# Performance work log

Hardware: AMD Instinct MI355X
Metric: run time of the kernel (lower is better)

Reference implementation:

```python
import jax, jax.numpy as jnp
import numpy as np

B, N, TD, SD, BD, K, M, TOPK, H = 8, 1024, 5120, 2048, 1024, 16, 4, 2, 8
HD = SD // H  # 256


def _ln(x, g, b, eps=1e-5):
    m = jnp.mean(x, -1, keepdims=True)
    v = jnp.mean((x - m) ** 2, -1, keepdims=True)
    return (x - m) * jax.lax.rsqrt(v + eps) * g + b


def _adapter(h, dw, db, uw, ub, lg, lb, q, wq, bq, wk, bk, wv, bv, ow, ob, pg, pb):
    # bottleneck trunk: down -> GELU -> up -> LN (dropout = identity in eval)
    x = jax.nn.gelu(h @ dw + db, approximate=False)          # [B,N,BD]
    x = _ln(x @ uw + ub, lg, lb)                             # [B,N,SD]
    Bb = x.shape[0]
    # cross-attention: learnable queries [K,SD] attend over x
    qp = (q @ wq + bq).reshape(K, H, HD).transpose(1, 0, 2)                      # [H,K,HD]
    kp = (x @ wk + bk).reshape(Bb, -1, H, HD).transpose(0, 2, 1, 3)              # [B,H,N,HD]
    vp = (x @ wv + bv).reshape(Bb, -1, H, HD).transpose(0, 2, 1, 3)              # [B,H,N,HD]
    att = jax.nn.softmax(jnp.einsum('hkd,bhnd->bhkn', qp, kp) * (1.0 / np.sqrt(HD)), axis=-1)
    ctx = jnp.einsum('bhkn,bhnd->bhkd', att, vp).transpose(0, 2, 1, 3).reshape(Bb, K, SD)
    ctx = ctx @ ow + ob
    return _ln(ctx + q[None], pg, pb)                        # residual with queries


def setup_inputs():
    key = jax.random.key(0)
    it = iter(jax.random.split(key, 40))
    def nrm(shape, s=0.02):
        return jax.random.normal(next(it), shape, jnp.float32) * s
    inp = {'h_teacher': jax.random.normal(next(it), (B, N, TD), jnp.float32)}
    for pre, lead in (('g_', ()), ('s_', (M,))):
        inp[pre + 'dw'] = nrm(lead + (TD, BD)); inp[pre + 'db'] = jnp.zeros(lead + (BD,), jnp.float32)
        inp[pre + 'uw'] = nrm(lead + (BD, SD)); inp[pre + 'ub'] = jnp.zeros(lead + (SD,), jnp.float32)
        inp[pre + 'lg'] = jnp.ones(lead + (SD,), jnp.float32); inp[pre + 'lb'] = jnp.zeros(lead + (SD,), jnp.float32)
        inp[pre + 'q'] = nrm(lead + (K, SD))
        for nm in ('wq', 'wk', 'wv', 'ow'):
            inp[pre + nm] = nrm(lead + (SD, SD))
        for nm in ('bq', 'bk', 'bv', 'ob'):
            inp[pre + nm] = jnp.zeros(lead + (SD,), jnp.float32)
        inp[pre + 'pg'] = jnp.ones(lead + (SD,), jnp.float32); inp[pre + 'pb'] = jnp.zeros(lead + (SD,), jnp.float32)
    inp['r_w1'] = nrm((TD, 512)); inp['r_b1'] = jnp.zeros((512,), jnp.float32)
    inp['r_w2'] = nrm((512, M)); inp['r_b2'] = jnp.zeros((M,), jnp.float32)
    return inp


def reference(h_teacher, g_dw, g_db, g_uw, g_ub, g_lg, g_lb, g_q, g_wq, g_bq, g_wk, g_bk, g_wv, g_bv, g_ow, g_ob, g_pg, g_pb, s_dw, s_db, s_uw, s_ub, s_lg, s_lb, s_q, s_wq, s_bq, s_wk, s_bk, s_wv, s_bv, s_ow, s_ob, s_pg, s_pb, r_w1, r_b1, r_w2, r_b2):
    # generalized adapter (always on)
    c_g = _adapter(h_teacher, g_dw, g_db, g_uw, g_ub, g_lg, g_lb, g_q, g_wq, g_bq, g_wk, g_bk, g_wv, g_bv, g_ow, g_ob, g_pg, g_pb)
    # all specialized experts computed densely (as the torch module does), then gathered
    c_spec = jax.vmap(lambda dw, db, uw, ub, lg, lb, q, wq, bq, wk, bk, wv, bv, ow, ob, pg, pb:
                      _adapter(h_teacher, dw, db, uw, ub, lg, lb, q, wq, bq, wk, bk, wv, bv, ow, ob, pg, pb))(
        s_dw, s_db, s_uw, s_ub, s_lg, s_lb, s_q, s_wq, s_bq, s_wk, s_bk, s_wv, s_bv, s_ow, s_ob, s_pg, s_pb)  # [M,B,K,SD]
    cs = jnp.transpose(c_spec, (1, 0, 2, 3))                 # [B,M,K,SD]
    # router on mean-pooled teacher summary (eval: no noise)
    pooled = jnp.mean(h_teacher, axis=1)                     # [B,TD]
    logits = jax.nn.gelu(pooled @ r_w1 + r_b1, approximate=False) @ r_w2 + r_b2
    probs = jax.nn.softmax(logits, axis=-1)                  # [B,M]
    w, idx = jax.lax.top_k(probs, TOPK)                      # [B,TOPK]
    w = w / (jnp.sum(w, -1, keepdims=True) + 1e-8)
    sel = cs[jnp.arange(cs.shape[0])[:, None], idx]          # [B,TOPK,K,SD]
    c_s = jnp.sum(sel * w[:, :, None, None], axis=1)         # [B,K,SD]
    c_agg = jnp.concatenate([c_g, c_s], axis=1)              # [B,2K,SD]
    return c_agg, probs
```

## Files before the change

### kernel.cpp

```cpp
#include <hip/hip_runtime.h>
#include <hip/hip_bf16.h>

#define B_   8
#define N_   1024
#define TD_  5120
#define SD_  2048
#define BD_  1024
#define K_   16
#define H_   8

typedef unsigned short u16;
typedef __attribute__((ext_vector_type(8))) short bf16x8;
typedef __attribute__((ext_vector_type(4))) float f32x4;
typedef __attribute__((ext_vector_type(8))) u16 u16x8;
typedef __attribute__((ext_vector_type(4))) u16 u16x4;

__device__ __forceinline__ float bf2f(u16 u) {
    union { unsigned int i; float f; } x; x.i = ((unsigned)u) << 16; return x.f;
}
__device__ __forceinline__ u16 f2bf(float f) {
    union { float f; unsigned int i; } x; x.f = f;
    unsigned int i = x.i;
    return (u16)((i + 0x7fffu + ((i >> 16) & 1u)) >> 16);
}
__device__ __forceinline__ float gelu_exact(float v) {
    return 0.5f * v * (1.0f + erff(v * 0.70710678118654752f));
}
__device__ __forceinline__ void gload_lds16(const void* g, void* l) {
    __builtin_amdgcn_global_load_lds(
        (const __attribute__((address_space(1))) unsigned int*)g,
        (__attribute__((address_space(3))) unsigned int*)l, 16, 0, 0);
}

struct Ptr5 { const float* p[5]; };
struct Ptr40 { const float* p[8][5]; };

template<int EPI, int AMODE>
__global__ __launch_bounds__(256, 4)
void gemm128(const u16* __restrict__ Abase,
             const u16* __restrict__ Bbase, long bStride,
             const float* __restrict__ biasBase, int biasStride,
             u16* __restrict__ Cbase, int ldc, long cStride, int Kd,
             const int* __restrict__ units_a, const int* __restrict__ units_b)
{
    __shared__ char lds[32768];
    const int u = blockIdx.z;
    const int ua = units_a[u];
    const int ub = (AMODE == 0) ? units_b[u] : u;
    const u16* A  = Abase + (size_t)ub * 1024 * Kd;
    const u16* Bt = Bbase + (size_t)ua * bStride;
    const float* bias = biasBase + (size_t)ua * biasStride;
    u16* C = Cbase + (size_t)u * cStride;

    const int tid  = threadIdx.x;
    const int wave = tid >> 6, lane = tid & 63;
    const int wm = wave >> 1, wn = wave & 1;
    const int row0 = blockIdx.x * 128, col0 = blockIdx.y * 128;

    const int srow = tid >> 3;
    const int scol = ((tid & 7) ^ (srow & 7)) << 3;
    const char* aSrc = (const char*)(A  + (size_t)(row0 + srow) * Kd + scol);
    const char* bSrc = (const char*)(Bt + (size_t)(col0 + srow) * Kd + scol);
    const int ldsW = wave * 1024;

    const int fr = lane & 15, fq = lane >> 4;
    const int kl  = fq << 4;
    const int swz = (fr & 7) << 4;

    f32x4 acc[4][4] = {};

#define LDA_(mf, kk) (*(const bf16x8*)(lds + \
    (wm*64 + (mf)*16 + fr)*128 + ((((kk)*64) + kl) ^ swz)))
#define LDB_(nf, kk) (*(const bf16x8*)(lds + 16384 + \
    (wn*64 + (nf)*16 + fr)*128 + ((((kk)*64) + kl) ^ swz)))

    const int nt = Kd >> 6;
    for (int T = 0; T < nt; ++T) {
        const size_t kb = (size_t)T << 7;
#pragma unroll
        for (int l = 0; l < 4; ++l)
            gload_lds16(aSrc + (size_t)(l*32)*Kd*2 + kb, lds + l*4096 + ldsW);
#pragma unroll
        for (int l = 0; l < 4; ++l)
            gload_lds16(bSrc + (size_t)(l*32)*Kd*2 + kb, lds + 16384 + l*4096 + ldsW);
        asm volatile("s_waitcnt vmcnt(0)" ::: "memory");
        __syncthreads();
#pragma unroll
        for (int kk = 0; kk < 2; ++kk) {
            bf16x8 aF[4], bF[4];
#pragma unroll
            for (int i = 0; i < 4; ++i) aF[i] = LDA_(i, kk);
#pragma unroll
            for (int n = 0; n < 4; ++n) bF[n] = LDB_(n, kk);
#pragma unroll
            for (int i = 0; i < 4; ++i)
#pragma unroll
                for (int n = 0; n < 4; ++n)
                    acc[i][n] = __builtin_amdgcn_mfma_f32_16x16x32_bf16(
                        aF[i], bF[n], acc[i][n], 0, 0, 0);
        }
        __syncthreads();
    }

#undef LDA_
#undef LDB_

#pragma unroll
    for (int mf = 0; mf < 4; ++mf)
#pragma unroll
        for (int nf = 0; nf < 4; ++nf) {
            const int col = col0 + wn*64 + nf*16 + fr;
            const float bv = bias[col];
#pragma unroll
            for (int j = 0; j < 4; ++j) {
                const int row = row0 + wm*64 + mf*16 + fq*4 + j;
                float v = acc[mf][nf][j] + bv;
                if (EPI == 1) v = gelu_exact(v);
                C[(size_t)row*ldc + col] = f2bf(v);
            }
        }
}

template<int EPI, int AMODE>
__global__ __launch_bounds__(512, 2)
void gemm256(const u16* __restrict__ Abase,
             const u16* __restrict__ Bbase, long bStride,
             const float* __restrict__ biasBase, int biasStride,
             u16* __restrict__ Cbase, int ldc, long cStride, int Kd,
             const int* __restrict__ units_a, const int* __restrict__ units_b)
{
    __shared__ char lds[131072];
    const int u = blockIdx.z;
    const int ua = units_a[u];
    const int ub = (AMODE == 0) ? units_b[u] : u;
    const u16* A  = Abase + (size_t)ub * 1024 * Kd;
    const u16* Bt = Bbase + (size_t)ua * bStride;
    const float* bias = biasBase + (size_t)ua * biasStride;
    u16* C = Cbase + (size_t)u * cStride;

    const int tid  = threadIdx.x;
    const int wave = tid >> 6, lane = tid & 63;
    const int wm = wave >> 2, wn = wave & 3;
    const int row0 = blockIdx.x * 256, col0 = blockIdx.y * 256;

    const int srow = tid >> 3;
    const int scol = ((tid & 7) ^ ((tid >> 3) & 7)) << 3;
    const char* aSrc = (const char*)(A  + (size_t)(row0 + srow) * Kd + scol);
    const char* bSrc = (const char*)(Bt + (size_t)(col0 + srow) * Kd + scol);
    const int ldsW = wave * 1024;

    const int fr = lane & 15, fq = lane >> 4;
    const int kl  = fq << 4;
    const int swz = (fr & 7) << 4;

    f32x4 acc[8][4] = {};
    bf16x8 aF[8], bF[4];

#define STAGE_A(bufv, hh, kt) do { \
    const char* s_ = aSrc + ((size_t)((hh)*128) * Kd + (size_t)(kt) * 64) * 2; \
    char* d_ = lds + (bufv)*65536 + (hh)*16384 + ldsW; \
    gload_lds16(s_, d_); \
    gload_lds16(s_ + (size_t)64 * Kd * 2, d_ + 8192); } while(0)
#define STAGE_B(bufv, hh, kt) do { \
    const char* s_ = bSrc + ((size_t)((hh)*128) * Kd + (size_t)(kt) * 64) * 2; \
    char* d_ = lds + (bufv)*65536 + 32768 + (hh)*16384 + ldsW; \
    gload_lds16(s_, d_); \
    gload_lds16(s_ + (size_t)64 * Kd * 2, d_ + 8192); } while(0)

#define LDA_(bufv, mf, kk) (*(const bf16x8*)(lds + (bufv)*65536 + \
    ((mf)*32 + wm*16 + fr)*128 + ((((kk)*64) + kl) ^ swz)))
#define LDB_(bufv, nf, kk) (*(const bf16x8*)(lds + (bufv)*65536 + 32768 + \
    (wn*64 + (nf)*16 + fr)*128 + ((((kk)*64) + kl) ^ swz)))

#define FENCE_ asm volatile("" ::: "memory")
#define BAR_   __builtin_amdgcn_s_barrier()
#define WAITL_ asm volatile("s_waitcnt lgkmcnt(0)" ::: "memory")
#define VM_(n) asm volatile("s_waitcnt vmcnt(" #n ")" ::: "memory")

#define READ_B(bufv, kk) { _Pragma("unroll") \
    for (int n_ = 0; n_ < 4; ++n_) bF[n_] = LDB_(bufv, n_, kk); }
#define READ_A8(bufv, kk) { _Pragma("unroll") \
    for (int i_ = 0; i_ < 8; ++i_) aF[i_] = LDA_(bufv, i_, kk); }
#define MFMA32_ { __builtin_amdgcn_s_setprio(1); \
    _Pragma("unroll") for (int i_ = 0; i_ < 8; ++i_) { \
      _Pragma("unroll") for (int n_ = 0; n_ < 4; ++n_) \
        acc[i_][n_] = __builtin_amdgcn_mfma_f32_16x16x32_bf16( \
            aF[i_], bF[n_], acc[i_][n_], 0, 0, 0); } \
    __builtin_amdgcn_s_setprio(0); }

    STAGE_A(0, 0, 0); STAGE_A(0, 1, 0);
    STAGE_B(0, 0, 0); STAGE_B(0, 1, 0);

    const int nt = Kd >> 6;
    for (int T = 0; T < nt - 1; ++T) {
        const int bufv = T & 1, nb = bufv ^ 1;
        STAGE_A(nb, 0, T + 1); STAGE_A(nb, 1, T + 1);
        VM_(4); BAR_; FENCE_;
        READ_B(bufv, 0); READ_A8(bufv, 0);
        STAGE_B(nb, 0, T + 1); STAGE_B(nb, 1, T + 1);
        WAITL_; MFMA32_;
        READ_B(bufv, 1); READ_A8(bufv, 1);
        WAITL_; MFMA32_;
        BAR_;
    }
    {
        const int bufv = (nt - 1) & 1;
        VM_(0); BAR_; FENCE_;
        READ_B(bufv, 0); READ_A8(bufv, 0);
        WAITL_; MFMA32_;
        READ_B(bufv, 1); READ_A8(bufv, 1);
        WAITL_; MFMA32_;
    }

#undef STAGE_A
#undef STAGE_B
#undef LDA_
#undef LDB_
#undef FENCE_
#undef BAR_
#undef WAITL_
#undef VM_
#undef READ_B
#undef READ_A8
#undef MFMA32_

#pragma unroll
    for (int mf = 0; mf < 8; ++mf)
#pragma unroll
        for (int nf = 0; nf < 4; ++nf) {
            const int col = col0 + wn*64 + nf*16 + fr;
            const float bv = bias[col];
#pragma unroll
            for (int j = 0; j < 4; ++j) {
                const int row = row0 + mf*32 + wm*16 + fq*4 + j;
                float v = acc[mf][nf][j] + bv;
                if (EPI == 1) v = gelu_exact(v);
                C[(size_t)row*ldc + col] = f2bf(v);
            }
        }
}

__global__ __launch_bounds__(256)
void cvt_pool(const float* __restrict__ h, u16* __restrict__ hb,
              float* __restrict__ pp) {
    const int b = blockIdx.x, nc = blockIdx.y, t = threadIdx.x;
    const float* hp = h + ((size_t)b*N_ + (size_t)nc*8)*TD_;
    u16* op = hb + ((size_t)b*N_ + (size_t)nc*8)*TD_;
    f32x4 sum[5] = {};
    for (int r = 0; r < 8; ++r) {
        const float* rp = hp + (size_t)r*TD_;
        u16* orow = op + (size_t)r*TD_;
#pragma unroll
        for (int j = 0; j < 5; ++j) {
            const int c = (t + 256*j) << 2;
            f32x4 v = *(const f32x4*)(rp + c);
            sum[j] += v;
            u16x4 o = { f2bf(v[0]), f2bf(v[1]), f2bf(v[2]), f2bf(v[3]) };
            *(u16x4*)(orow + c) = o;
        }
    }
#pragma unroll
    for (int j = 0; j < 5; ++j) {
        const int c = (t + 256*j) << 2;
        *(f32x4*)(pp + ((size_t)b*128 + nc)*TD_ + c) = sum[j];
    }
}

__global__ void pool_reduce(const float* __restrict__ pp, float* __restrict__ pooled) {
    const int idx = blockIdx.x*256 + threadIdx.x;
    const int b = idx / TD_, c = idx % TD_;
    float s = 0.f;
    for (int nc = 0; nc < 128; ++nc) s += pp[((size_t)b*128 + nc)*TD_ + c];
    pooled[idx] = s * (1.0f/N_);
}

__global__ __launch_bounds__(256)
void cvt_transpose5(Ptr5 W5, u16* __restrict__ WtBase, long wtStride,
                    int Kd, int Nd) {
    __shared__ float t[64][65];
    const float* W = W5.p[blockIdx.z];
    u16* Wt = WtBase + (size_t)blockIdx.z * wtStride;
    const int k0 = blockIdx.x * 64, n0 = blockIdx.y * 64;
    const int tid = threadIdx.x;
#pragma unroll
    for (int i = 0; i < 4; ++i) {
        int ch = tid + i*256;
        int r = ch >> 4, c4 = (ch & 15) << 2;
        f32x4 v = *(const f32x4*)(W + (size_t)(k0 + r)*Nd + n0 + c4);
        t[r][c4] = v[0]; t[r][c4+1] = v[1]; t[r][c4+2] = v[2]; t[r][c4+3] = v[3];
    }
    __syncthreads();
#pragma unroll
    for (int i = 0; i < 2; ++i) {
        int ch = tid + i*256;
        int nr = ch >> 3, c8 = (ch & 7) << 3;
        u16x8 o;
#pragma unroll
        for (int j = 0; j < 8; ++j) o[j] = f2bf(t[c8 + j][nr]);
        *(u16x8*)(Wt + (size_t)(n0 + nr)*Kd + k0 + c8) = o;
    }
}

__global__ __launch_bounds__(256)
void ln_rows_u(u16* __restrict__ X, const float* __restrict__ gslab,
               const float* __restrict__ bslab, const int* __restrict__ units_a) {
    const int row = blockIdx.x, tid = threadIdx.x;
    const int ua = units_a[row >> 10];
    const float* g  = gslab + (size_t)ua*SD_;
    const float* bt = bslab + (size_t)ua*SD_;
    u16* rp = X + (size_t)row*SD_;
    const u16x8 v = ((const u16x8*)rp)[tid];
    float f[8]; float s = 0.f, s2 = 0.f;
#pragma unroll
    for (int j = 0; j < 8; ++j) { f[j] = bf2f(v[j]); s += f[j]; s2 += f[j]*f[j]; }
    __shared__ float sa[4], sb[4];
#pragma unroll
    for (int o = 32; o > 0; o >>= 1) { s += __shfl_down(s, o); s2 += __shfl_down(s2, o); }
    if ((tid & 63) == 0) { sa[tid >> 6] = s; sb[tid >> 6] = s2; }
    __syncthreads();
    s = sa[0]+sa[1]+sa[2]+sa[3]; s2 = sb[0]+sb[1]+sb[2]+sb[3];
    const float mean = s * (1.0f/SD_);
    const float inv  = rsqrtf(s2 * (1.0f/SD_) - mean*mean + 1e-5f);
    const int c0 = tid*8;
    u16x8 o;
#pragma unroll
    for (int j = 0; j < 8; ++j) o[j] = f2bf((f[j]-mean)*inv*g[c0+j] + bt[c0+j]);
    ((u16x8*)rp)[tid] = o;
}

__global__ __launch_bounds__(256)
void qp_part(Ptr5 q, Ptr5 wq, float* __restrict__ Sp) {
    __shared__ float qL[16][256];
    const int a = blockIdx.y, ks = blockIdx.z;
    const int c = blockIdx.x*256 + threadIdx.x;
    const int t = threadIdx.x;
    const float* Q = q.p[a];
    for (int i = t; i < 16*256; i += 256)
        qL[i >> 8][i & 255] = Q[(size_t)(i >> 8)*SD_ + ks*256 + (i & 255)];
    __syncthreads();
    const float* W = wq.p[a] + (size_t)(ks*256)*SD_ + c;
    float acc[16] = {};
    for (int i = 0; i < 256; i += 4) {
        const float w0 = W[(size_t)i*SD_];
        const float w1 = W[(size_t)(i+1)*SD_];
        const float w2 = W[(size_t)(i+2)*SD_];
        const float w3 = W[(size_t)(i+3)*SD_];
#pragma unroll
        for (int k = 0; k < 16; ++k) {
            f32x4 q4 = *(const f32x4*)&qL[k][i];
            acc[k] += q4[0]*w0 + q4[1]*w1 + q4[2]*w2 + q4[3]*w3;
        }
    }
#pragma unroll
    for (int k = 0; k < 16; ++k)
        Sp[((size_t)(a*8 + ks)*16 + k)*SD_ + c] = acc[k];
}

__global__ void qp_reduce(const float* __restrict__ Sp, Ptr5 bq, float* __restrict__ qp) {
    const int idx = blockIdx.x*256 + threadIdx.x;
    const int a = idx >> 15, k = (idx >> 11) & 15, c = idx & 2047;
    float s = bq.p[a][c];
#pragma unroll
    for (int ks = 0; ks < 8; ++ks)
        s += Sp[((size_t)(a*8 + ks)*16 + k)*SD_ + c];
    qp[idx] = s;
}

__global__ __launch_bounds__(256)
void scores_sm(const u16* __restrict__ Kb, const float* __restrict__ qp,
               const int* __restrict__ units_a, float* __restrict__ P)
{
    __shared__ float sL[16][1024];
    __shared__ float qL[16][256];
    __shared__ float red[8];
    const int u = blockIdx.x >> 3, hh = blockIdx.x & 7;
    const int ua = units_a[u];
    const int t = threadIdx.x;
    for (int i = t; i < 16*256; i += 256)
        qL[i >> 8][i & 255] = qp[(size_t)(ua*16 + (i >> 8))*SD_ + hh*256 + (i & 255)];
    __syncthreads();
    const u16* Ku = Kb + (size_t)u*1024*SD_ + hh*256;
#pragma unroll
    for (int j = 0; j < 4; ++j) {
        const int n = t + j*256;
        const u16* kr = Ku + (size_t)n*SD_;
        float acc[16] = {};
        for (int d0 = 0; d0 < 256; d0 += 8) {
            u16x8 kv8 = *(const u16x8*)(kr + d0);
            float kf[8];
#pragma unroll
            for (int e = 0; e < 8; ++e) kf[e] = bf2f(kv8[e]);
#pragma unroll
            for (int k = 0; k < 16; ++k) {
                f32x4 q0 = *(const f32x4*)&qL[k][d0];
                f32x4 q1 = *(const f32x4*)&qL[k][d0+4];
                acc[k] += q0[0]*kf[0] + q0[1]*kf[1] + q0[2]*kf[2] + q0[3]*kf[3]
                        + q1[0]*kf[4] + q1[1]*kf[5] + q1[2]*kf[6] + q1[3]*kf[7];
            }
        }
#pragma unroll
        for (int k = 0; k < 16; ++k) sL[k][n] = acc[k] * 0.0625f;
    }
    __syncthreads();
    const int lane = t & 63, wv = t >> 6;
    for (int k = 0; k < 16; ++k) {
        float v0 = sL[k][t], v1 = sL[k][t+256], v2 = sL[k][t+512], v3 = sL[k][t+768];
        float mx = fmaxf(fmaxf(v0,v1), fmaxf(v2,v3));
#pragma unroll
        for (int o = 1; o < 64; o <<= 1) mx = fmaxf(mx, __shfl_xor(mx, o));
        if (lane == 0) red[wv] = mx;
        __syncthreads();
        mx = fmaxf(fmaxf(red[0],red[1]), fmaxf(red[2],red[3]));
        float e0 = expf(v0-mx), e1 = expf(v1-mx), e2 = expf(v2-mx), e3 = expf(v3-mx);
        float s = e0+e1+e2+e3;
#pragma unroll
        for (int o = 1; o < 64; o <<= 1) s += __shfl_xor(s, o);
        if (lane == 0) red[4+wv] = s;
        __syncthreads();
        s = red[4]+red[5]+red[6]+red[7];
        const float inv = 1.0f/s;
        float* Pr = P + ((size_t)(u*8+hh)*16 + k)*1024;
        Pr[t]=e0*inv; Pr[t+256]=e1*inv; Pr[t+512]=e2*inv; Pr[t+768]=e3*inv;
        __syncthreads();
    }
}

__global__ __launch_bounds__(256)
void ctx_u(const u16* __restrict__ Vb, const float* __restrict__ P,
           u16* __restrict__ ctxb)
{
    __shared__ float pL[16][1024];
    const int u = blockIdx.x >> 3, hh = blockIdx.x & 7;
    const int t = threadIdx.x;
    const float* Pu = P + (size_t)(u*8+hh)*16*1024;
    for (int i = t; i < 16*1024/4; i += 256)
        ((f32x4*)&pL[0][0])[i] = ((const f32x4*)Pu)[i];
    __syncthreads();
    const u16* Vu = Vb + (size_t)u*1024*SD_ + hh*256 + t;
    float acc[16] = {};
    for (int n = 0; n < 1024; n += 4) {
        float vv0 = bf2f(Vu[(size_t)n*SD_]);
        float vv1 = bf2f(Vu[(size_t)(n+1)*SD_]);
        float vv2 = bf2f(Vu[(size_t)(n+2)*SD_]);
        float vv3 = bf2f(Vu[(size_t)(n+3)*SD_]);
#pragma unroll
        for (int k = 0; k < 16; ++k) {
            f32x4 p4 = *(const f32x4*)&pL[k][n];
            acc[k] += p4[0]*vv0 + p4[1]*vv1 + p4[2]*vv2 + p4[3]*vv3;
        }
    }
#pragma unroll
    for (int k = 0; k < 16; ++k)
        ctxb[(size_t)u*16*SD_ + k*SD_ + hh*256 + t] = f2bf(acc[k]);
}

__global__ __launch_bounds__(256)
void gemm_ow_part(const u16* __restrict__ ctxb, const u16* __restrict__ Bslab,
                  const int* __restrict__ units_a, float* __restrict__ ctx2p)
{
    const int u = blockIdx.y, ua = units_a[u], ks = blockIdx.z;
    const int wave = threadIdx.x >> 6, lane = threadIdx.x & 63;
    const int col0 = blockIdx.x*256 + wave*64;
    const u16* A  = ctxb + (size_t)u*16*SD_;
    const u16* Bt = Bslab + (size_t)ua*SD_*SD_;
    const int fr = lane & 15, fk8 = (lane >> 4) << 3;
    f32x4 acc[4] = {};
    const int kbase = ks*512;
    for (int k0 = kbase; k0 < kbase + 512; k0 += 32) {
        bf16x8 af = *(const bf16x8*)(A + (size_t)fr*SD_ + k0 + fk8);
#pragma unroll
        for (int n = 0; n < 4; ++n) {
            bf16x8 bf8 = *(const bf16x8*)(Bt + (size_t)(col0 + n*16 + fr)*SD_ + k0 + fk8);
            acc[n] = __builtin_amdgcn_mfma_f32_16x16x32_bf16(af, bf8, acc[n], 0, 0, 0);
        }
    }
    const int fq = lane >> 4;
#pragma unroll
    for (int n = 0; n < 4; ++n)
#pragma unroll
        for (int j = 0; j < 4; ++j) {
            const int row = fq*4 + j, col = col0 + n*16 + fr;
            ctx2p[(((size_t)ks*24 + u)*16 + row)*SD_ + col] = acc[n][j];
        }
}

__global__ void gemm_ow_reduce(const float* __restrict__ ctx2p,
                               const float* __restrict__ biasSlab,
                               const int* __restrict__ units_a,
                               float* __restrict__ ctx2) {
    const int idx = blockIdx.x*256 + threadIdx.x;
    const int u = idx / (16*SD_);
    const int rem = idx % (16*SD_);
    const int col = rem % SD_;
    float s = biasSlab[units_a[u]*SD_ + col];
#pragma unroll
    for (int ks = 0; ks < 4; ++ks)
        s += ctx2p[((size_t)ks*24*16*SD_) + (size_t)u*16*SD_ + rem];
    ctx2[idx] = s;
}

__global__ __launch_bounds__(256)
void ln_post_u(const float* __restrict__ ctx2, const float* __restrict__ qslab,
               const float* __restrict__ pgs, const float* __restrict__ pbs,
               const int* __restrict__ units_a, const int* __restrict__ units_b,
               float* __restrict__ out, float* __restrict__ cspec)
{
    const int k = blockIdx.x, u = blockIdx.y, tid = threadIdx.x;
    const int ua = units_a[u];
    const float* ip = ctx2 + ((size_t)u*16 + k)*SD_;
    const float* qr = qslab + ((size_t)ua*16 + k)*SD_;
    const float* g  = pgs + (size_t)ua*SD_;
    const float* bt = pbs + (size_t)ua*SD_;
    float f[8]; float s = 0.f, s2 = 0.f;
#pragma unroll
    for (int j = 0; j < 8; ++j) {
        const int c = tid + j*256;
        f[j] = ip[c] + qr[c];
        s += f[j]; s2 += f[j]*f[j];
    }
    __shared__ float sa[4], sb[4];
#pragma unroll
    for (int o = 32; o > 0; o >>= 1) { s += __shfl_down(s, o); s2 += __shfl_down(s2, o); }
    if ((tid & 63) == 0) { sa[tid >> 6] = s; sb[tid >> 6] = s2; }
    __syncthreads();
    s = sa[0]+sa[1]+sa[2]+sa[3]; s2 = sb[0]+sb[1]+sb[2]+sb[3];
    const float mean = s * (1.0f/SD_);
    const float inv  = rsqrtf(s2 * (1.0f/SD_) - mean*mean + 1e-5f);
    float* op = (u < 8) ? out + ((size_t)units_b[u]*32 + k)*SD_
                        : cspec + ((size_t)(u-8)*16 + k)*SD_;
#pragma unroll
    for (int j = 0; j < 8; ++j) { const int c = tid + j*256; op[c] = (f[j]-mean)*inv*g[c] + bt[c]; }
}

__global__ __launch_bounds__(256)
void rmlp_part(const float* __restrict__ pooled, const float* __restrict__ w1,
               float* __restrict__ rp) {
    const int c = blockIdx.x*256 + threadIdx.x;
    const int b = blockIdx.y, is = blockIdx.z;
    const float* pr = pooled + b*TD_ + is*512;
    const float* W = w1 + (size_t)(is*512)*512 + c;
    float s = 0.f;
    for (int i = 0; i < 512; ++i) s += pr[i] * W[(size_t)i*512];
    rp[(b*10 + is)*512 + c] = s;
}
__global__ void rmlp_reduce(const float* __restrict__ rp, const float* __restrict__ b1,
                            float* __restrict__ hid) {
    const int idx = blockIdx.x*256 + threadIdx.x;
    const int b = idx >> 9, c = idx & 511;
    float s = b1[c];
#pragma unroll
    for (int is = 0; is < 10; ++is) s += rp[(b*10 + is)*512 + c];
    hid[idx] = gelu_exact(s);
}

__global__ void router_final(const float* __restrict__ hid, const float* __restrict__ w2,
                             const float* __restrict__ b2, float* __restrict__ probs,
                             int* __restrict__ widx, float* __restrict__ wval,
                             int* __restrict__ units_a, int* __restrict__ units_b) {
    __shared__ float lg[8][4];
    __shared__ int sw[16];
    const int tid = threadIdx.x;
    if (tid < 32) {
        const int b = tid >> 2, m = tid & 3;
        float s = b2[m];
        const float* hr = hid + b*512;
        for (int i = 0; i < 512; ++i) s += hr[i]*w2[i*4 + m];
        lg[b][m] = s;
    }
    __syncthreads();
    if (tid < 8) {
        const int b = tid;
        const float l0=lg[b][0], l1=lg[b][1], l2=lg[b][2], l3=lg[b][3];
        const float mx = fmaxf(fmaxf(l0,l1),fmaxf(l2,l3));
        const float e0=expf(l0-mx), e1=expf(l1-mx), e2=expf(l2-mx), e3=expf(l3-mx);
        const float s = e0+e1+e2+e3;
        float p[4] = {e0/s, e1/s, e2/s, e3/s};
        probs[b*4+0]=p[0]; probs[b*4+1]=p[1]; probs[b*4+2]=p[2]; probs[b*4+3]=p[3];
        int i0 = 0;
        for (int m = 1; m < 4; ++m) if (p[m] > p[i0]) i0 = m;
        int i1 = -1;
        for (int m = 0; m < 4; ++m) if (m != i0 && (i1 < 0 || p[m] > p[i1])) i1 = m;
        const float w0 = p[i0], w1 = p[i1], ws = w0 + w1 + 1e-8f;
        widx[b*2]=i0; widx[b*2+1]=i1;
        wval[b*2]=w0/ws; wval[b*2+1]=w1/ws;
        sw[b*2]=i0; sw[b*2+1]=i1;
    }
    __syncthreads();
    if (tid < 24) {
        units_a[tid] = (tid < 8) ? 0 : sw[tid-8] + 1;
        units_b[tid] = (tid < 8) ? tid : ((tid-8) >> 1);
    }
}

__global__ void combine_k(const float* __restrict__ cspec, const int* __restrict__ widx,
                          const float* __restrict__ wval, float* __restrict__ out) {
    const int i = blockIdx.x*256 + threadIdx.x;
    const int c4 = i & 511;
    const int k  = (i >> 9) & 15;
    const int b  = i >> 13;
    const float w0 = wval[b*2], w1 = wval[b*2+1];
    const f32x4 v0 = ((const f32x4*)cspec)[(size_t)((2*b)  *16 + k)*512 + c4];
    const f32x4 v1 = ((const f32x4*)cspec)[(size_t)((2*b+1)*16 + k)*512 + c4];
    ((f32x4*)out)[(size_t)(b*32 + 16 + k)*512 + c4] = v0*w0 + v1*w1;
}

__global__ void pack5(Ptr5 src, float* __restrict__ dst, int len) {
    int i = blockIdx.x*256 + threadIdx.x;
    if (i < 5*len) dst[i] = src.p[i/len][i%len];
}
__global__ void pack_slab8(Ptr40 s, float* __restrict__ dst) {
    int i = blockIdx.x*256 + threadIdx.x;
    int slab = i / 10240, rem = i % 10240;
    dst[i] = s.p[slab][rem / 2048][rem % 2048];
}

extern "C" void kernel_launch(void* const* d_in, const int* in_sizes, int n_in,
                              void* d_out, int out_size, void* d_ws, size_t ws_size,
                              hipStream_t stream) {
    if (ws_size < 300300000ULL) return;

    const float* h = (const float*)d_in[0];
    const float* G[17]; const float* Sx[17];
    for (int i = 0; i < 17; ++i) { G[i] = (const float*)d_in[1+i]; Sx[i] = (const float*)d_in[18+i]; }
    const float* r_w1 = (const float*)d_in[35];
    const float* r_b1 = (const float*)d_in[36];
    const float* r_w2 = (const float*)d_in[37];
    const float* r_b2 = (const float*)d_in[38];

    static const size_t str[17] = {
        (size_t)TD_*BD_, BD_, (size_t)BD_*SD_, SD_, SD_, SD_, (size_t)K_*SD_,
        (size_t)SD_*SD_, (size_t)SD_*SD_, (size_t)SD_*SD_, (size_t)SD_*SD_,
        SD_, SD_, SD_, SD_, SD_, SD_ };
    auto P = [&](int pi, int a) -> const float* {
        return (a == 0) ? G[pi] : Sx[pi] + (size_t)(a-1)*str[pi];
    };

    char* w = (char*)d_ws;
    const size_t R0 = 0, R1 = 100663296, R2 = 201326592, R3 = 251658240, TAIL = 293601280;
    u16*   h_bf  = (u16*)(w + R0);
    u16*   X     = (u16*)(w + R0);
    u16*   wt_dw = (u16*)(w + R1);
    u16*   Kbuf  = (u16*)(w + R1);
    u16*   X1    = (u16*)(w + R2);
    u16*   wt_v  = (u16*)(w + R2);
    u16*   wt_ow = (u16*)(w + R2);
    u16*   wt_uw = (u16*)(w + R3);
    u16*   wt_k  = (u16*)(w + R3);
    u16*   ctxb  = (u16*)(w + R3);
    float* ctx2  = (float*)(w + R3 + 1572864);
    float* cspec = (float*)(w + R3 + 4718592);
    float* Pbuf  = (float*)(w + R3 + 6815744);
    float* ctx2p = (float*)(w + R3 + 19398656);
    float* qpp   = (float*)(w + R2);
    float* poolp = (float*)(w + R2 + 12582912);
    float* routp = (float*)(w + R2 + 33554432);
    float* qp_all  = (float*)(w + TAIL);
    float* qslab   = (float*)(w + TAIL + 655360);
    float* bias_dw = (float*)(w + TAIL + 1310720);
    float* slab8   = (float*)(w + TAIL + 1331200);
    float* pooled  = (float*)(w + TAIL + 1658880);
    float* hid     = (float*)(w + TAIL + 1822720);
    int*   widx    = (int*)  (w + TAIL + 1839104);
    float* wval    = (float*)(w + TAIL + 1839168);
    int*   units_a = (int*)  (w + TAIL + 1839232);
    int*   units_b = (int*)  (w + TAIL + 1839328);

    float* bias_uw = slab8;
    float* bias_k  = slab8 + 1*5*SD_;
    float* bias_v  = slab8 + 2*5*SD_;
    float* bias_ow = slab8 + 3*5*SD_;
    float* lng     = slab8 + 4*5*SD_;
    float* lnb     = slab8 + 5*5*SD_;
    float* pgs     = slab8 + 6*5*SD_;
    float* pbs     = slab8 + 7*5*SD_;

    float* out = (float*)d_out;

    cvt_pool<<<dim3(8, 128), 256, 0, stream>>>(h, h_bf, poolp);
    pool_reduce<<<160, 256, 0, stream>>>(poolp, pooled);
    rmlp_part<<<dim3(2, 8, 10), 256, 0, stream>>>(pooled, r_w1, routp);
    rmlp_reduce<<<16, 256, 0, stream>>>(routp, r_b1, hid);
    router_final<<<1, 64, 0, stream>>>(hid, r_w2, r_b2, out + 524288, widx, wval, units_a, units_b);

    Ptr5 q5, wq5, bq5, db5;
    for (int a = 0; a < 5; ++a) { q5.p[a]=P(6,a); wq5.p[a]=P(7,a); bq5.p[a]=P(11,a); db5.p[a]=P(1,a); }
    qp_part<<<dim3(8, 5, 8), 256, 0, stream>>>(q5, wq5, qpp);
    qp_reduce<<<640, 256, 0, stream>>>(qpp, bq5, qp_all);
    pack5<<<20, 256, 0, stream>>>(db5, bias_dw, BD_);
    pack5<<<640, 256, 0, stream>>>(q5, qslab, 16*SD_);
    Ptr40 s8;
    static const int slab_pi[8] = {3, 12, 13, 14, 4, 5, 15, 16};
    for (int si = 0; si < 8; ++si)
        for (int a = 0; a < 5; ++a) s8.p[si][a] = P(slab_pi[si], a);
    pack_slab8<<<320, 256, 0, stream>>>(s8, slab8);

    Ptr5 dw5, uw5, k5, v5, ow5;
    for (int a = 0; a < 5; ++a) {
        dw5.p[a] = P(0,a); uw5.p[a] = P(2,a);
        k5.p[a] = P(8,a); v5.p[a] = P(9,a); ow5.p[a] = P(10,a);
    }
    cvt_transpose5<<<dim3(TD_/64, BD_/64, 5), 256, 0, stream>>>(dw5, wt_dw, (long)BD_*TD_, TD_, BD_);
    cvt_transpose5<<<dim3(BD_/64, SD_/64, 5), 256, 0, stream>>>(uw5, wt_uw, (long)SD_*BD_, BD_, SD_);

    gemm128<1, 0><<<dim3(8, 8, 24), 256, 0, stream>>>(
        h_bf, wt_dw, (long)BD_*TD_, bias_dw, BD_, X1, BD_, (long)1024*BD_, TD_, units_a, units_b);

    gemm256<0, 1><<<dim3(4, 8, 24), 512, 0, stream>>>(
        X1, wt_uw, (long)SD_*BD_, bias_uw, SD_, X, SD_, (long)1024*SD_, BD_, units_a, units_b);

    ln_rows_u<<<24*1024, 256, 0, stream>>>(X, lng, lnb, units_a);

    cvt_transpose5<<<dim3(SD_/64, SD_/64, 5), 256, 0, stream>>>(k5, wt_k, (long)SD_*SD_, SD_, SD_);
    cvt_transpose5<<<dim3(SD_/64, SD_/64, 5), 256, 0, stream>>>(v5, wt_v, (long)SD_*SD_, SD_, SD_);

    gemm256<0, 1><<<dim3(4, 8, 24), 512, 0, stream>>>(
        X, wt_k, (long)SD_*SD_, bias_k, SD_, Kbuf, SD_, (long)1024*SD_, SD_, units_a, units_b);

    scores_sm<<<24*8, 256, 0, stream>>>(Kbuf, qp_all, units_a, Pbuf);

    gemm256<0, 1><<<dim3(4, 8, 24), 512, 0, stream>>>(
        X, wt_v, (long)SD_*SD_, bias_v, SD_, Kbuf, SD_, (long)1024*SD_, SD_, units_a, units_b);

    cvt_transpose5<<<dim3(SD_/64, SD_/64, 5), 256, 0, stream>>>(ow5, wt_ow, (long)SD_*SD_, SD_, SD_);

    ctx_u<<<24*8, 256, 0, stream>>>(Kbuf, Pbuf, ctxb);

    gemm_ow_part<<<dim3(8, 24, 4), 256, 0, stream>>>(ctxb, wt_ow, units_a, ctx2p);
    gemm_ow_reduce<<<3072, 256, 0, stream>>>(ctx2p, bias_ow, units_a, ctx2);

    ln_post_u<<<dim3(16, 24), 256, 0, stream>>>(ctx2, qslab, pgs, pbs, units_a, units_b, out, cspec);
    combine_k<<<256, 256, 0, stream>>>(cspec, widx, wval, out);
}
```

Baseline: 1.319 ms.

## Replace double-buffered 256x256 GEMM pipeline with single-buffer synchronous loop

The 256x256 GEMM used for up-projection, K and V projections drops its two-stage LDS double buffer and interleaved prefetch/MFMA schedule. It now uses one 64KB LDS buffer: each K-tile loads fully, waits on vmcnt(0), syncs, computes, then syncs again. Halving LDS may let more blocks fit per CU, but global-load latency is no longer hidden behind MFMA work and the setprio hints are gone.

```diff
diff --git a/kernel.cpp b/kernel.cpp
--- a/kernel.cpp
+++ b/kernel.cpp
@@ -123,13 +123,13 @@
 
 template<int EPI, int AMODE>
 __global__ __launch_bounds__(512, 2)
-void gemm256(const u16* __restrict__ Abase,
-             const u16* __restrict__ Bbase, long bStride,
-             const float* __restrict__ biasBase, int biasStride,
-             u16* __restrict__ Cbase, int ldc, long cStride, int Kd,
-             const int* __restrict__ units_a, const int* __restrict__ units_b)
+void gemm256s(const u16* __restrict__ Abase,
+              const u16* __restrict__ Bbase, long bStride,
+              const float* __restrict__ biasBase, int biasStride,
+              u16* __restrict__ Cbase, int ldc, long cStride, int Kd,
+              const int* __restrict__ units_a, const int* __restrict__ units_b)
 {
-    __shared__ char lds[131072];
+    __shared__ char lds[65536];
     const int u = blockIdx.z;
     const int ua = units_a[u];
     const int ub = (AMODE == 0) ? units_b[u] : u;
@@ -144,7 +144,7 @@
     const int row0 = blockIdx.x * 256, col0 = blockIdx.y * 256;
 
     const int srow = tid >> 3;
-    const int scol = ((tid & 7) ^ ((tid >> 3) & 7)) << 3;
+    const int scol = ((tid & 7) ^ (srow & 7)) << 3;
     const char* aSrc = (const char*)(A  + (size_t)(row0 + srow) * Kd + scol);
     const char* bSrc = (const char*)(Bt + (size_t)(col0 + srow) * Kd + scol);
     const int ldsW = wave * 1024;
@@ -154,75 +154,42 @@
     const int swz = (fr & 7) << 4;
 
     f32x4 acc[8][4] = {};
-    bf16x8 aF[8], bF[4];
-
-#define STAGE_A(bufv, hh, kt) do { \
-    const char* s_ = aSrc + ((size_t)((hh)*128) * Kd + (size_t)(kt) * 64) * 2; \
-    char* d_ = lds + (bufv)*65536 + (hh)*16384 + ldsW; \
-    gload_lds16(s_, d_); \
-    gload_lds16(s_ + (size_t)64 * Kd * 2, d_ + 8192); } while(0)
-#define STAGE_B(bufv, hh, kt) do { \
-    const char* s_ = bSrc + ((size_t)((hh)*128) * Kd + (size_t)(kt) * 64) * 2; \
-    char* d_ = lds + (bufv)*65536 + 32768 + (hh)*16384 + ldsW; \
-    gload_lds16(s_, d_); \
-    gload_lds16(s_ + (size_t)64 * Kd * 2, d_ + 8192); } while(0)
-
-#define LDA_(bufv, mf, kk) (*(const bf16x8*)(lds + (bufv)*65536 + \
+
+#define LDA_(mf, kk) (*(const bf16x8*)(lds + \
     ((mf)*32 + wm*16 + fr)*128 + ((((kk)*64) + kl) ^ swz)))
-#define LDB_(bufv, nf, kk) (*(const bf16x8*)(lds + (bufv)*65536 + 32768 + \
+#define LDB_(nf, kk) (*(const bf16x8*)(lds + 32768 + \
     (wn*64 + (nf)*16 + fr)*128 + ((((kk)*64) + kl) ^ swz)))
 
-#define FENCE_ asm volatile("" ::: "memory")
-#define BAR_   __builtin_amdgcn_s_barrier()
-#define WAITL_ asm volatile("s_waitcnt lgkmcnt(0)" ::: "memory")
-#define VM_(n) asm volatile("s_waitcnt vmcnt(" #n ")" ::: "memory")
-
-#define READ_B(bufv, kk) { _Pragma("unroll") \
-    for (int n_ = 0; n_ < 4; ++n_) bF[n_] = LDB_(bufv, n_, kk); }
-#define READ_A8(bufv, kk) { _Pragma("unroll") \
-    for (int i_ = 0; i_ < 8; ++i_) aF[i_] = LDA_(bufv, i_, kk); }
-#define MFMA32_ { __builtin_amdgcn_s_setprio(1); \
-    _Pragma("unroll") for (int i_ = 0; i_ < 8; ++i_) { \
-      _Pragma("unroll") for (int n_ = 0; n_ < 4; ++n_) \
-        acc[i_][n_] = __builtin_amdgcn_mfma_f32_16x16x32_bf16( \
-            aF[i_], bF[n_], acc[i_][n_], 0, 0, 0); } \
-    __builtin_amdgcn_s_setprio(0); }
-
-    STAGE_A(0, 0, 0); STAGE_A(0, 1, 0);
-    STAGE_B(0, 0, 0); STAGE_B(0, 1, 0);
-
     const int nt = Kd >> 6;
-    for (int T = 0; T < nt - 1; ++T) {
-        const int bufv = T & 1, nb = bufv ^ 1;
-        STAGE_A(nb, 0, T + 1); STAGE_A(nb, 1, T + 1);
-        VM_(4); BAR_; FENCE_;
-        READ_B(bufv, 0); READ_A8(bufv, 0);
-        STAGE_B(nb, 0, T + 1); STAGE_B(nb, 1, T + 1);
-        WAITL_; MFMA32_;
-        READ_B(bufv, 1); READ_A8(bufv, 1);
-        WAITL_; MFMA32_;
-        BAR_;
-    }
-    {
-        const int bufv = (nt - 1) & 1;
-        VM_(0); BAR_; FENCE_;
-        READ_B(bufv, 0); READ_A8(bufv, 0);
-        WAITL_; MFMA32_;
-        READ_B(bufv, 1); READ_A8(bufv, 1);
-        WAITL_; MFMA32_;
-    }
-
-#undef STAGE_A
-#undef STAGE_B
+    for (int T = 0; T < nt; ++T) {
+        const size_t kb = (size_t)T << 7;
+#pragma unroll
+        for (int l = 0; l < 4; ++l)
+            gload_lds16(aSrc + (size_t)(l*64)*Kd*2 + kb, lds + l*8192 + ldsW);
+#pragma unroll
+        for (int l = 0; l < 4; ++l)
+            gload_lds16(bSrc + (size_t)(l*64)*Kd*2 + kb, lds + 32768 + l*8192 + ldsW);
+        asm volatile("s_waitcnt vmcnt(0)" ::: "memory");
+        __syncthreads();
+#pragma unroll
+        for (int kk = 0; kk < 2; ++kk) {
+            bf16x8 aF[8], bF[4];
+#pragma unroll
+            for (int n = 0; n < 4; ++n) bF[n] = LDB_(n, kk);
+#pragma unroll
+            for (int i = 0; i < 8; ++i) aF[i] = LDA_(i, kk);
+#pragma unroll
+            for (int i = 0; i < 8; ++i)
+#pragma unroll
+                for (int n = 0; n < 4; ++n)
+                    acc[i][n] = __builtin_amdgcn_mfma_f32_16x16x32_bf16(
+                        aF[i], bF[n], acc[i][n], 0, 0, 0);
+        }
+        __syncthreads();
+    }
+
 #undef LDA_
 #undef LDB_
-#undef FENCE_
-#undef BAR_
-#undef WAITL_
-#undef VM_
-#undef READ_B
-#undef READ_A8
-#undef MFMA32_
 
 #pragma unroll
     for (int mf = 0; mf < 8; ++mf)
@@ -705,7 +672,7 @@
     gemm128<1, 0><<<dim3(8, 8, 24), 256, 0, stream>>>(
         h_bf, wt_dw, (long)BD_*TD_, bias_dw, BD_, X1, BD_, (long)1024*BD_, TD_, units_a, units_b);
 
-    gemm256<0, 1><<<dim3(4, 8, 24), 512, 0, stream>>>(
+    gemm256s<0, 1><<<dim3(4, 8, 24), 512, 0, stream>>>(
         X1, wt_uw, (long)SD_*BD_, bias_uw, SD_, X, SD_, (long)1024*SD_, BD_, units_a, units_b);
 
     ln_rows_u<<<24*1024, 256, 0, stream>>>(X, lng, lnb, units_a);
@@ -713,12 +680,12 @@
     cvt_transpose5<<<dim3(SD_/64, SD_/64, 5), 256, 0, stream>>>(k5, wt_k, (long)SD_*SD_, SD_, SD_);
     cvt_transpose5<<<dim3(SD_/64, SD_/64, 5), 256, 0, stream>>>(v5, wt_v, (long)SD_*SD_, SD_, SD_);
 
-    gemm256<0, 1><<<dim3(4, 8, 24), 512, 0, stream>>>(
+    gemm256s<0, 1><<<dim3(4, 8, 24), 512, 0, stream>>>(
         X, wt_k, (long)SD_*SD_, bias_k, SD_, Kbuf, SD_, (long)1024*SD_, SD_, units_a, units_b);
 
     scores_sm<<<24*8, 256, 0, stream>>>(Kbuf, qp_all, units_a, Pbuf);
 
-    gemm256<0, 1><<<dim3(4, 8, 24), 512, 0, stream>>>(
+    gemm256s<0, 1><<<dim3(4, 8, 24), 512, 0, stream>>>(
         X, wt_v, (long)SD_*SD_, bias_v, SD_, Kbuf, SD_, (long)1024*SD_, SD_, units_a, units_b);
 
     cvt_transpose5<<<dim3(SD_/64, SD_/64, 5), 256, 0, stream>>>(ow5, wt_ow, (long)SD_*SD_, SD_, SD_);
```

Result: slower. 1.491 ms (+13.0%).
